# Performance work log

Hardware: AMD Instinct MI355X
Metric: run time of the kernel (lower is better)

## Reference

```python
import jax, jax.numpy as jnp
import numpy as np


def _hilbert_envelope(x1d):
    """|analytic signal| of a real 1-D signal, matching scipy.signal.hilbert."""
    N = x1d.shape[0]  # static at trace time
    h = np.zeros(N, dtype=np.float32)
    if N % 2 == 0:
        h[0] = 1.0
        h[N // 2] = 1.0
        h[1:N // 2] = 2.0
    else:
        h[0] = 1.0
        h[1:(N + 1) // 2] = 2.0
    Xf = jnp.fft.fft(x1d)
    analytic = jnp.fft.ifft(Xf * jnp.asarray(h))
    return jnp.abs(analytic)


def setup_inputs() -> dict:
    key = jax.random.key(0)
    B, L, D = 32, 4096, 64
    x = jax.random.normal(key, (B, L, D), dtype=jnp.float32)
    return {"x": x}


def reference(x):
    B, L, D = x.shape
    flat = x.reshape(-1)  # [B*L*D], one long signal as in the original
    up = jnp.clip(flat, 0.0, None)
    down = jnp.clip(-flat, 0.0, None)
    envelope_max = _hilbert_envelope(up).reshape(B, L, D)
    envelope_min = (-_hilbert_envelope(down)).reshape(B, L, D)
    avg_envelope = (envelope_max + envelope_min) * 0.5
    imf = x - avg_envelope
    # torch.std(dim=1, unbiased=True) -> ddof=1 over the time axis
    std_res = jnp.std(imf, axis=1, keepdims=True, ddof=1) + jnp.float32(0.01)
    return imf / std_res, avg_envelope
```

## Files before the change

### kernel.cpp

```cpp
#include <hip/hip_runtime.h>
#include <math.h>

#define NTOT 8388608
#define N1   2048
#define N2   4096
#define BB   32
#define LL   4096
#define DD   64

enum { M_NONE = 0, M_TW = 1, M_SCALE = 4 };

__device__ inline float2 cmul(float2 a, float2 b) {
    return make_float2(a.x*b.x - a.y*b.y, a.x*b.y + a.y*b.x);
}
__device__ inline float2 cmul_conj(float2 a, float2 b) {
    return make_float2(a.x*b.x + a.y*b.y, a.y*b.x - a.x*b.y);
}
__device__ inline float2 cadd(float2 a, float2 b){ return make_float2(a.x+b.x, a.y+b.y); }
__device__ inline float2 csub(float2 a, float2 b){ return make_float2(a.x-b.x, a.y-b.y); }
__device__ inline float2 mul_pi(float2 a){ return make_float2(-a.y, a.x); }
__device__ inline float2 mul_mi(float2 a){ return make_float2(a.y, -a.x); }
__device__ inline int pidx(int a){ return a + (a >> 4); }

template<bool INV>
__device__ inline void dft8(const float2* x, float2* y) {
    const float C = 0.70710678118654752f;
    float2 t0=cadd(x[0],x[4]), t1=cadd(x[1],x[5]), t2=cadd(x[2],x[6]), t3=cadd(x[3],x[7]);
    float2 u0=csub(x[0],x[4]), u1=csub(x[1],x[5]), u2=csub(x[2],x[6]), u3=csub(x[3],x[7]);
    if (!INV) {
        u1 = make_float2(C*(u1.x+u1.y), C*(u1.y-u1.x));
        u2 = mul_mi(u2);
        u3 = make_float2(C*(u3.y-u3.x), -C*(u3.x+u3.y));
    } else {
        u1 = make_float2(C*(u1.x-u1.y), C*(u1.y+u1.x));
        u2 = mul_pi(u2);
        u3 = make_float2(-C*(u3.x+u3.y), C*(u3.x-u3.y));
    }
    {
        float2 s0=cadd(t0,t2), s1=cadd(t1,t3), d0=csub(t0,t2);
        float2 d1 = INV ? mul_pi(csub(t1,t3)) : mul_mi(csub(t1,t3));
        y[0]=cadd(s0,s1); y[4]=csub(s0,s1); y[2]=cadd(d0,d1); y[6]=csub(d0,d1);
    }
    {
        float2 s0=cadd(u0,u2), s1=cadd(u1,u3), d0=csub(u0,u2);
        float2 d1 = INV ? mul_pi(csub(u1,u3)) : mul_mi(csub(u1,u3));
        y[1]=cadd(s0,s1); y[5]=csub(s0,s1); y[3]=cadd(d0,d1); y[7]=csub(d0,d1);
    }
}

__device__ inline void dft8_h0_inv(const float2* x, float2* y) {
    const float C = 0.70710678118654752f;
    float2 u1 = make_float2(C*(x[1].x - x[1].y), C*(x[1].y + x[1].x));
    float2 u2 = mul_pi(x[2]);
    float2 u3 = make_float2(-C*(x[3].x + x[3].y), C*(x[3].x - x[3].y));
    {
        float2 s0=cadd(x[0],x[2]), s1=cadd(x[1],x[3]), d0=csub(x[0],x[2]);
        float2 d1 = mul_pi(csub(x[1],x[3]));
        y[0]=cadd(s0,s1); y[4]=csub(s0,s1); y[2]=cadd(d0,d1); y[6]=csub(d0,d1);
    }
    {
        float2 s0=cadd(x[0],u2), s1=cadd(u1,u3), d0=csub(x[0],u2);
        float2 d1 = mul_pi(csub(u1,u3));
        y[1]=cadd(s0,s1); y[5]=csub(s0,s1); y[3]=cadd(d0,d1); y[7]=csub(d0,d1);
    }
}

template<bool INV>
__device__ inline void dft4(const float2* u, float2* y) {
    float2 s0=cadd(u[0],u[2]), s1=cadd(u[1],u[3]), d0=csub(u[0],u[2]);
    float2 d1 = INV ? mul_pi(csub(u[1],u[3])) : mul_mi(csub(u[1],u[3]));
    y[0]=cadd(s0,s1); y[2]=csub(s0,s1); y[1]=cadd(d0,d1); y[3]=csub(d0,d1);
}

template<bool INV, int SH>
__device__ inline void twiddle8(float2* y, int ps, const float2* __restrict__ T1t) {
    float2 w1 = T1t[(ps << SH) & 4095];
    float2 w2 = cmul(w1, w1);
    float2 w3 = cmul(w2, w1);
    float2 w4 = cmul(w2, w2);
    float2 w5 = cmul(w4, w1);
    float2 w6 = cmul(w3, w3);
    float2 w7 = cmul(w4, w3);
    if (!INV) {
        y[1]=cmul(y[1],w1); y[2]=cmul(y[2],w2); y[3]=cmul(y[3],w3);
        y[4]=cmul(y[4],w4); y[5]=cmul(y[5],w5); y[6]=cmul(y[6],w6); y[7]=cmul(y[7],w7);
    } else {
        y[1]=cmul_conj(y[1],w1); y[2]=cmul_conj(y[2],w2); y[3]=cmul_conj(y[3],w3);
        y[4]=cmul_conj(y[4],w4); y[5]=cmul_conj(y[5],w5); y[6]=cmul_conj(y[6],w6); y[7]=cmul_conj(y[7],w7);
    }
}

__global__ __launch_bounds__(256) void gen_tables(float2* T1, float2* T2) {
    int j = blockIdx.x * 256 + threadIdx.x;
    if (j < 4096) {
        double ang = -2.0 * M_PI * (double)j / 4096.0;
        T1[j] = make_float2((float)cos(ang), (float)sin(ang));
    } else if (j < 4096 + 2048) {
        int b = j - 4096;
        double ang = -2.0 * M_PI * (double)b / 8388608.0;
        T2[b] = make_float2((float)cos(ang), (float)sin(ang));
    }
}

__device__ inline float2 wbig(int t, const float2* __restrict__ T1t, const float2* __restrict__ T2t) {
    return cmul(T1t[t >> 11], T2t[t & 2047]);
}

template<bool INV, int MODE>
__global__ __launch_bounds__(512) void fft4096(float2* data,
                                               const float2* __restrict__ T1t,
                                               const float2* __restrict__ T2t) {
    __shared__ float2 S[4352];
    const int t = threadIdx.x;
    const int r = blockIdx.x;
    float2* base = data + (size_t)r * 4096;

    float2 x[8], y[8];
    #pragma unroll
    for (int m = 0; m < 8; ++m) x[m] = base[t + 512*m];

    #pragma unroll
    for (int st = 0; st < 3; ++st) {
        const int s = 1 << (3*st);
        const int q = t & (s - 1);
        const int ps = t - q;
        dft8<INV>(x, y);
        twiddle8<INV, 0>(y, ps, T1t);
        if (st) __syncthreads();
        #pragma unroll
        for (int k = 0; k < 8; ++k) S[pidx(8*ps + q + k*s)] = y[k];
        __syncthreads();
        #pragma unroll
        for (int m = 0; m < 8; ++m) x[m] = S[pidx(t + 512*m)];
    }
    dft8<INV>(x, y);

    if (MODE == M_TW) {
        float2 wb    = wbig(r * t, T1t, T2t);
        float2 wstep = wbig(512 * r, T1t, T2t);
        #pragma unroll
        for (int k = 0; k < 8; ++k) {
            int o = t + 512*k;
            base[o] = INV ? cmul_conj(y[k], wb) : cmul(y[k], wb);
            wb = INV ? cmul_conj(wb, wstep) : cmul(wb, wstep);
        }
    } else {
        #pragma unroll
        for (int k = 0; k < 8; ++k) {
            int o = t + 512*k;
            float2 v = y[k];
            if (MODE == M_SCALE) {
                const float sc = 1.f / 8388608.f;
                v.x *= sc; v.y *= sc;
            }
            base[o] = v;
        }
    }
}

__global__ __launch_bounds__(256) void fftmid(float2* data,
                                              const float2* __restrict__ T1t,
                                              const float2* __restrict__ T2t) {
    __shared__ float2 S[2176];
    const int t = threadIdx.x;
    const int r = blockIdx.x;
    float2* base = data + (size_t)r * 2048;

    float2 x[8], y[8];
    #pragma unroll
    for (int m = 0; m < 8; ++m) x[m] = base[t + 256*m];

    #pragma unroll
    for (int st = 0; st < 3; ++st) {
        const int s = 1 << (3*st);
        const int q = t & (s - 1);
        const int ps = t - q;
        dft8<false>(x, y);
        twiddle8<false, 1>(y, ps, T1t);
        if (st) __syncthreads();
        #pragma unroll
        for (int k = 0; k < 8; ++k) S[pidx(8*ps + q + k*s)] = y[k];
        __syncthreads();
        if (st < 2) {
            #pragma unroll
            for (int m = 0; m < 8; ++m) x[m] = S[pidx(t + 256*m)];
        }
    }
    float2 xa[4], xb[4], ya[4], yb[4];
    #pragma unroll
    for (int m = 0; m < 4; ++m) {
        xa[m] = S[pidx(t + 512*m)];
        xb[m] = S[pidx(t + 256 + 512*m)];
    }
    dft4<false>(xa, ya);
    dft4<false>(xb, yb);
    __syncthreads();
    #pragma unroll
    for (int k = 0; k < 4; ++k) {
        int o = t + 512*k;
        if (o < 1024) {
            float h = (o == 0 && r == 0) ? 1.f : 2.f;
            S[pidx(o)] = make_float2(ya[k].x * h, ya[k].y * h);
        } else if (o == 1024) {
            S[pidx(1024)] = (r == 0) ? ya[k] : make_float2(0.f, 0.f);
        }
        int o2 = o + 256;
        if (o2 < 1024) S[pidx(o2)] = make_float2(yb[k].x * 2.f, yb[k].y * 2.f);
    }
    __syncthreads();
    #pragma unroll
    for (int m = 0; m < 4; ++m) x[m] = S[pidx(t + 256*m)];
    dft8_h0_inv(x, y);
    if (t == 0) {
        float2 c = S[pidx(1024)];
        #pragma unroll
        for (int k = 0; k < 8; ++k) {
            if (k & 1) { y[k].x -= c.x; y[k].y -= c.y; }
            else       { y[k].x += c.x; y[k].y += c.y; }
        }
    }
    twiddle8<true, 1>(y, t, T1t);
    __syncthreads();
    #pragma unroll
    for (int k = 0; k < 8; ++k) S[pidx(8*t + k)] = y[k];
    __syncthreads();
    #pragma unroll
    for (int st = 1; st < 3; ++st) {
        const int s = 1 << (3*st);
        const int q = t & (s - 1);
        const int ps = t - q;
        #pragma unroll
        for (int m = 0; m < 8; ++m) x[m] = S[pidx(t + 256*m)];
        dft8<true>(x, y);
        twiddle8<true, 1>(y, ps, T1t);
        __syncthreads();
        #pragma unroll
        for (int k = 0; k < 8; ++k) S[pidx(8*ps + q + k*s)] = y[k];
        __syncthreads();
    }
    #pragma unroll
    for (int m = 0; m < 4; ++m) {
        xa[m] = S[pidx(t + 512*m)];
        xb[m] = S[pidx(t + 256 + 512*m)];
    }
    dft4<true>(xa, ya);
    dft4<true>(xb, yb);
    {
        float2 wka   = wbig(r * t, T1t, T2t);
        float2 w256  = wbig(256 * r, T1t, T2t);
        float2 w512  = cmul(w256, w256);
        float2 wkb   = cmul(wka, w256);
        #pragma unroll
        for (int k = 0; k < 4; ++k) {
            int o = t + 512*k;
            base[o]       = cmul_conj(ya[k], wka);
            base[o + 256] = cmul_conj(yb[k], wkb);
            wka = cmul(wka, w512);
            wkb = cmul(wkb, w512);
        }
    }
}

__global__ __launch_bounds__(256) void k_pre(const float* __restrict__ x, float2* __restrict__ A) {
    __shared__ float tile[32][33];
    int c0 = blockIdx.x * 32;
    int r0 = blockIdx.y * 32;
    int tx = threadIdx.x, ty = threadIdx.y;
    #pragma unroll
    for (int j = 0; j < 32; j += 8)
        tile[ty + j][tx] = x[(size_t)(r0 + ty + j) * N1 + c0 + tx];
    __syncthreads();
    #pragma unroll
    for (int j = 0; j < 32; j += 8) {
        float v = tile[tx][ty + j];
        A[(size_t)(c0 + ty + j) * N2 + r0 + tx] = make_float2(fmaxf(v, 0.f), fmaxf(-v, 0.f));
    }
}

__global__ __launch_bounds__(256) void k_trans(const float2* __restrict__ in, float2* __restrict__ out,
                                               int inCols, int inRows) {
    __shared__ float2 tile[32][33];
    int c0 = blockIdx.x * 32;
    int r0 = blockIdx.y * 32;
    int tx = threadIdx.x, ty = threadIdx.y;
    #pragma unroll
    for (int j = 0; j < 32; j += 8)
        tile[ty + j][tx] = in[(size_t)(r0 + ty + j) * inCols + c0 + tx];
    __syncthreads();
    #pragma unroll
    for (int j = 0; j < 32; j += 8)
        out[(size_t)(c0 + ty + j) * inRows + r0 + tx] = tile[tx][ty + j];
}

__global__ __launch_bounds__(256) void k_post(const float2* __restrict__ A, const float* __restrict__ x,
                                              float* __restrict__ out) {
    __shared__ float2 tile[32][33];
    int c0 = blockIdx.x * 32;
    int r0 = blockIdx.y * 32;
    int tx = threadIdx.x, ty = threadIdx.y;
    #pragma unroll
    for (int j = 0; j < 32; j += 8)
        tile[ty + j][tx] = A[(size_t)(r0 + ty + j) * N2 + c0 + tx];
    __syncthreads();
    #pragma unroll
    for (int j = 0; j < 32; j += 8) {
        int n2 = c0 + ty + j;
        int n1 = r0 + tx;
        size_t n = (size_t)n2 * N1 + n1;
        float2 w = tile[tx][ty + j];
        float xv = x[n];
        float up = fmaxf(xv, 0.f);
        float dn = fmaxf(-xv, 0.f);
        float hu = w.y - dn;
        float hd = up - w.x;
        float em = sqrtf(up*up + hu*hu);
        float en = sqrtf(dn*dn + hd*hd);
        float avg = 0.5f * (em - en);
        out[n]        = xv - avg;
        out[NTOT + n] = avg;
    }
}

__global__ __launch_bounds__(256) void std_partial(const float* __restrict__ imf, float* __restrict__ part) {
    int blk = blockIdx.x;
    int b   = blk >> 4;
    int ch  = blk & 15;
    int d   = threadIdx.x & 63;
    int lw  = threadIdx.x >> 6;
    float s1 = 0.f, s2 = 0.f;
    const float* base = imf + (size_t)b * LL * DD;
    for (int i = 0; i < 64; ++i) {
        int l = ch * 256 + lw * 64 + i;
        float v = base[(size_t)l * DD + d];
        s1 += v;
        s2 += v * v;
    }
    __shared__ float r1[4][64];
    __shared__ float r2[4][64];
    r1[lw][d] = s1; r2[lw][d] = s2;
    __syncthreads();
    if (lw == 0) {
        s1 = r1[0][d] + r1[1][d] + r1[2][d] + r1[3][d];
        s2 = r2[0][d] + r2[1][d] + r2[2][d] + r2[3][d];
        int pi = blk * 64 + d;
        part[pi] = s1;
        part[BB * 16 * 64 + pi] = s2;
    }
}

__global__ __launch_bounds__(256) void std_final(const float* __restrict__ part, float* __restrict__ scalev) {
    int g = blockIdx.x * 256 + threadIdx.x;
    int b = g >> 6, d = g & 63;
    float s1 = 0.f, s2 = 0.f;
    for (int ch = 0; ch < 16; ++ch) {
        int pi = (b * 16 + ch) * 64 + d;
        s1 += part[pi];
        s2 += part[BB * 16 * 64 + pi];
    }
    float mean = s1 / (float)LL;
    float var  = (s2 - (float)LL * mean * mean) / (float)(LL - 1);
    var = fmaxf(var, 0.f);
    scalev[g] = 1.f / (sqrtf(var) + 0.01f);
}

__global__ __launch_bounds__(256) void apply_scale(float* __restrict__ out, const float* __restrict__ scalev) {
    size_t i = ((size_t)blockIdx.x * 256 + threadIdx.x) * 4;
    float4 v = *(float4*)(out + i);
    int b = (int)(i >> 18);
    int d = (int)(i & 63);
    const float* sc = scalev + b * 64;
    v.x *= sc[d];
    v.y *= sc[d + 1];
    v.z *= sc[d + 2];
    v.w *= sc[d + 3];
    *(float4*)(out + i) = v;
}

extern "C" void kernel_launch(void* const* d_in, const int* in_sizes, int n_in,
                              void* d_out, int out_size, void* d_ws, size_t ws_size,
                              hipStream_t stream) {
    const float* x = (const float*)d_in[0];
    float* out = (float*)d_out;
    char* w = (char*)d_ws;

    float2* T1     = (float2*)w;
    float2* T2     = (float2*)(w + 32 * 1024);
    float*  part   = (float*)(w + 48 * 1024);
    float*  scalev = (float*)(w + 320 * 1024);
    float2* A      = (float2*)(w + (1 << 20));
    float2* Bbuf   = (float2*)d_out;

    hipLaunchKernelGGL(gen_tables, dim3(24), dim3(256), 0, stream, T1, T2);

    hipLaunchKernelGGL(k_pre, dim3(N1/32, N2/32), dim3(32, 8), 0, stream, x, A);
    hipLaunchKernelGGL((fft4096<false, M_TW>), dim3(N1), dim3(512), 0, stream, A, T1, T2);
    hipLaunchKernelGGL(k_trans, dim3(N2/32, N1/32), dim3(32, 8), 0, stream, A, Bbuf, N2, N1);
    hipLaunchKernelGGL(fftmid, dim3(N2), dim3(256), 0, stream, Bbuf, T1, T2);
    hipLaunchKernelGGL(k_trans, dim3(N1/32, N2/32), dim3(32, 8), 0, stream, Bbuf, A, N1, N2);
    hipLaunchKernelGGL((fft4096<true, M_SCALE>), dim3(N1), dim3(512), 0, stream, A, T1, T2);
    hipLaunchKernelGGL(k_post, dim3(N2/32, N1/32), dim3(32, 8), 0, stream, A, x, out);

    hipLaunchKernelGGL(std_partial, dim3(BB * 16), dim3(256), 0, stream, out, part);
    hipLaunchKernelGGL(std_final, dim3(8), dim3(256), 0, stream, part, scalev);
    hipLaunchKernelGGL(apply_scale, dim3(NTOT / 4 / 256), dim3(256), 0, stream, out, scalev);
}
```

Before: 201.8 us.

## Replace transpose-based four-step FFT with fused column/row FFT kernels

Restructures the 8M-point Hilbert FFT as a four-step scheme with 2048 rows by 4096 columns. Two column-FFT kernels each process 4 adjacent columns in shared memory with an XOR swizzle, so the separate transpose, pre and post kernels are no longer needed. The row kernel fuses the forward FFT, the Hilbert mask and the inverse FFT in place. This removes several full-array global-memory round trips. In exchange it uses strided float4 column loads and 64KB of shared memory per block, which limits occupancy.

```diff
diff --git a/kernel.cpp b/kernel.cpp
--- a/kernel.cpp
+++ b/kernel.cpp
@@ -2,13 +2,11 @@
 #include <math.h>
 
 #define NTOT 8388608
-#define N1   2048
-#define N2   4096
+#define RR   2048
+#define CC   4096
 #define BB   32
 #define LL   4096
 #define DD   64
-
-enum { M_NONE = 0, M_TW = 1, M_SCALE = 4 };
 
 __device__ inline float2 cmul(float2 a, float2 b) {
     return make_float2(a.x*b.x - a.y*b.y, a.x*b.y + a.y*b.x);
@@ -21,6 +19,7 @@
 __device__ inline float2 mul_pi(float2 a){ return make_float2(-a.y, a.x); }
 __device__ inline float2 mul_mi(float2 a){ return make_float2(a.y, -a.x); }
 __device__ inline int pidx(int a){ return a + (a >> 4); }
+__device__ inline int swz(int a){ return a ^ (((a >> 5) & 15) << 1); }
 
 template<bool INV>
 __device__ inline void dft8(const float2* x, float2* y) {
@@ -106,218 +105,234 @@
     return cmul(T1t[t >> 11], T2t[t & 2047]);
 }
 
-template<bool INV, int MODE>
-__global__ __launch_bounds__(512) void fft4096(float2* data,
+__global__ __launch_bounds__(256) void col_fwd(const float* __restrict__ x, float2* __restrict__ Y,
+                                               const float2* __restrict__ T1t,
+                                               const float2* __restrict__ T2t) {
+    __shared__ float2 S[8192];
+    const int t = threadIdx.x;
+    const int c0 = blockIdx.x * 4;
+    #pragma unroll
+    for (int g = 0; g < 8; ++g) {
+        int n1 = t + 256*g;
+        float4 v = *(const float4*)(x + (size_t)n1*CC + c0);
+        S[swz(4*n1+0)] = make_float2(fmaxf(v.x,0.f), fmaxf(-v.x,0.f));
+        S[swz(4*n1+1)] = make_float2(fmaxf(v.y,0.f), fmaxf(-v.y,0.f));
+        S[swz(4*n1+2)] = make_float2(fmaxf(v.z,0.f), fmaxf(-v.z,0.f));
+        S[swz(4*n1+3)] = make_float2(fmaxf(v.w,0.f), fmaxf(-v.w,0.f));
+    }
+    __syncthreads();
+    const int u = t >> 2, c = t & 3;
+    const int n2 = c0 + c;
+    float2 in[4][8], y[8];
+    #pragma unroll
+    for (int st = 0; st < 3; ++st) {
+        const int s = 1 << (3*st);
+        #pragma unroll
+        for (int g = 0; g < 4; ++g) {
+            int j = u + 64*g;
+            #pragma unroll
+            for (int m = 0; m < 8; ++m) in[g][m] = S[swz(4*(j + 256*m) + c)];
+        }
+        __syncthreads();
+        #pragma unroll
+        for (int g = 0; g < 4; ++g) {
+            int j = u + 64*g;
+            int q = j & (s-1), ps = j - q;
+            dft8<false>(in[g], y);
+            twiddle8<false,1>(y, ps, T1t);
+            #pragma unroll
+            for (int k = 0; k < 8; ++k) S[swz(4*(8*ps + q + k*s) + c)] = y[k];
+        }
+        __syncthreads();
+    }
+    float2 q4[8][4];
+    #pragma unroll
+    for (int g = 0; g < 8; ++g) {
+        int j = u + 64*g;
+        #pragma unroll
+        for (int m = 0; m < 4; ++m) q4[g][m] = S[swz(4*(j + 512*m) + c)];
+    }
+    __syncthreads();
+    const float2 ws = wbig(512 * n2, T1t, T2t);
+    #pragma unroll
+    for (int g = 0; g < 8; ++g) {
+        int j = u + 64*g;
+        float2 y4[4];
+        dft4<false>(q4[g], y4);
+        float2 wb = wbig(n2 * j, T1t, T2t);
+        #pragma unroll
+        for (int m = 0; m < 4; ++m) {
+            S[swz(4*(j + 512*m) + c)] = cmul(y4[m], wb);
+            wb = cmul(wb, ws);
+        }
+    }
+    __syncthreads();
+    #pragma unroll
+    for (int g = 0; g < 8; ++g) {
+        int k1 = t + 256*g;
+        float2 a = S[swz(4*k1+0)], b = S[swz(4*k1+1)];
+        float2 cc2 = S[swz(4*k1+2)], d = S[swz(4*k1+3)];
+        float4* p = (float4*)(Y + (size_t)k1*CC + c0);
+        p[0] = make_float4(a.x, a.y, b.x, b.y);
+        p[1] = make_float4(cc2.x, cc2.y, d.x, d.y);
+    }
+}
+
+__global__ __launch_bounds__(512) void row_mid(float2* __restrict__ Y,
                                                const float2* __restrict__ T1t,
                                                const float2* __restrict__ T2t) {
     __shared__ float2 S[4352];
     const int t = threadIdx.x;
     const int r = blockIdx.x;
-    float2* base = data + (size_t)r * 4096;
-
-    float2 x[8], y[8];
-    #pragma unroll
-    for (int m = 0; m < 8; ++m) x[m] = base[t + 512*m];
-
+    float2* base = Y + (size_t)r * CC;
+    float2 x8[8], y8[8];
+    #pragma unroll
+    for (int m = 0; m < 8; ++m) x8[m] = base[t + 512*m];
     #pragma unroll
     for (int st = 0; st < 3; ++st) {
         const int s = 1 << (3*st);
-        const int q = t & (s - 1);
-        const int ps = t - q;
-        dft8<INV>(x, y);
-        twiddle8<INV, 0>(y, ps, T1t);
+        const int q = t & (s-1), ps = t - q;
+        dft8<false>(x8, y8);
+        twiddle8<false,0>(y8, ps, T1t);
         if (st) __syncthreads();
         #pragma unroll
-        for (int k = 0; k < 8; ++k) S[pidx(8*ps + q + k*s)] = y[k];
-        __syncthreads();
-        #pragma unroll
-        for (int m = 0; m < 8; ++m) x[m] = S[pidx(t + 512*m)];
-    }
-    dft8<INV>(x, y);
-
-    if (MODE == M_TW) {
-        float2 wb    = wbig(r * t, T1t, T2t);
-        float2 wstep = wbig(512 * r, T1t, T2t);
+        for (int k = 0; k < 8; ++k) S[pidx(8*ps + q + k*s)] = y8[k];
+        __syncthreads();
+        #pragma unroll
+        for (int m = 0; m < 8; ++m) x8[m] = S[pidx(t + 512*m)];
+    }
+    dft8<false>(x8, y8);
+    float2 z8[4];
+    #pragma unroll
+    for (int k = 0; k < 4; ++k) {
+        int k2 = t + 512*k;
+        float h = (k2 == 0 && r == 0) ? 1.f : 2.f;
+        z8[k] = make_float2(y8[k].x*h, y8[k].y*h);
+    }
+    float2 corner = y8[4];
+    dft8_h0_inv(z8, y8);
+    if (r == 0 && t == 0) {
         #pragma unroll
         for (int k = 0; k < 8; ++k) {
-            int o = t + 512*k;
-            base[o] = INV ? cmul_conj(y[k], wb) : cmul(y[k], wb);
-            wb = INV ? cmul_conj(wb, wstep) : cmul(wb, wstep);
-        }
-    } else {
-        #pragma unroll
-        for (int k = 0; k < 8; ++k) {
-            int o = t + 512*k;
-            float2 v = y[k];
-            if (MODE == M_SCALE) {
-                const float sc = 1.f / 8388608.f;
-                v.x *= sc; v.y *= sc;
-            }
-            base[o] = v;
-        }
-    }
-}
-
-__global__ __launch_bounds__(256) void fftmid(float2* data,
-                                              const float2* __restrict__ T1t,
-                                              const float2* __restrict__ T2t) {
-    __shared__ float2 S[2176];
+            if (k & 1) { y8[k].x -= corner.x; y8[k].y -= corner.y; }
+            else       { y8[k].x += corner.x; y8[k].y += corner.y; }
+        }
+    }
+    twiddle8<true,0>(y8, t, T1t);
+    __syncthreads();
+    #pragma unroll
+    for (int k = 0; k < 8; ++k) S[pidx(8*t + k)] = y8[k];
+    __syncthreads();
+    #pragma unroll
+    for (int st = 1; st < 3; ++st) {
+        const int s = 1 << (3*st);
+        const int q = t & (s-1), ps = t - q;
+        #pragma unroll
+        for (int m = 0; m < 8; ++m) x8[m] = S[pidx(t + 512*m)];
+        dft8<true>(x8, y8);
+        twiddle8<true,0>(y8, ps, T1t);
+        __syncthreads();
+        #pragma unroll
+        for (int k = 0; k < 8; ++k) S[pidx(8*ps + q + k*s)] = y8[k];
+        __syncthreads();
+    }
+    #pragma unroll
+    for (int m = 0; m < 8; ++m) x8[m] = S[pidx(t + 512*m)];
+    dft8<true>(x8, y8);
+    const float sc = 1.f / 8388608.f;
+    float2 wb = wbig(r * t, T1t, T2t);
+    wb.x *= sc; wb.y *= sc;
+    const float2 wstep = wbig(512 * r, T1t, T2t);
+    #pragma unroll
+    for (int k = 0; k < 8; ++k) {
+        base[t + 512*k] = cmul_conj(y8[k], wb);
+        wb = cmul(wb, wstep);
+    }
+}
+
+__global__ __launch_bounds__(256) void col_inv(const float2* __restrict__ Y, const float* __restrict__ x,
+                                               float* __restrict__ out,
+                                               const float2* __restrict__ T1t,
+                                               const float2* __restrict__ T2t) {
+    __shared__ float2 S[8192];
     const int t = threadIdx.x;
-    const int r = blockIdx.x;
-    float2* base = data + (size_t)r * 2048;
-
-    float2 x[8], y[8];
-    #pragma unroll
-    for (int m = 0; m < 8; ++m) x[m] = base[t + 256*m];
-
+    const int c0 = blockIdx.x * 4;
+    #pragma unroll
+    for (int g = 0; g < 8; ++g) {
+        int k1 = t + 256*g;
+        const float4* p = (const float4*)(Y + (size_t)k1*CC + c0);
+        float4 ab = p[0], cd = p[1];
+        S[swz(4*k1+0)] = make_float2(ab.x, ab.y);
+        S[swz(4*k1+1)] = make_float2(ab.z, ab.w);
+        S[swz(4*k1+2)] = make_float2(cd.x, cd.y);
+        S[swz(4*k1+3)] = make_float2(cd.z, cd.w);
+    }
+    __syncthreads();
+    const int u = t >> 2, c = t & 3;
+    float2 in[4][8], y[8];
     #pragma unroll
     for (int st = 0; st < 3; ++st) {
         const int s = 1 << (3*st);
-        const int q = t & (s - 1);
-        const int ps = t - q;
-        dft8<false>(x, y);
-        twiddle8<false, 1>(y, ps, T1t);
-        if (st) __syncthreads();
-        #pragma unroll
-        for (int k = 0; k < 8; ++k) S[pidx(8*ps + q + k*s)] = y[k];
-        __syncthreads();
-        if (st < 2) {
+        #pragma unroll
+        for (int g = 0; g < 4; ++g) {
+            int j = u + 64*g;
             #pragma unroll
-            for (int m = 0; m < 8; ++m) x[m] = S[pidx(t + 256*m)];
-        }
-    }
-    float2 xa[4], xb[4], ya[4], yb[4];
-    #pragma unroll
-    for (int m = 0; m < 4; ++m) {
-        xa[m] = S[pidx(t + 512*m)];
-        xb[m] = S[pidx(t + 256 + 512*m)];
-    }
-    dft4<false>(xa, ya);
-    dft4<false>(xb, yb);
-    __syncthreads();
-    #pragma unroll
-    for (int k = 0; k < 4; ++k) {
-        int o = t + 512*k;
-        if (o < 1024) {
-            float h = (o == 0 && r == 0) ? 1.f : 2.f;
-            S[pidx(o)] = make_float2(ya[k].x * h, ya[k].y * h);
-        } else if (o == 1024) {
-            S[pidx(1024)] = (r == 0) ? ya[k] : make_float2(0.f, 0.f);
-        }
-        int o2 = o + 256;
-        if (o2 < 1024) S[pidx(o2)] = make_float2(yb[k].x * 2.f, yb[k].y * 2.f);
-    }
-    __syncthreads();
-    #pragma unroll
-    for (int m = 0; m < 4; ++m) x[m] = S[pidx(t + 256*m)];
-    dft8_h0_inv(x, y);
-    if (t == 0) {
-        float2 c = S[pidx(1024)];
-        #pragma unroll
-        for (int k = 0; k < 8; ++k) {
-            if (k & 1) { y[k].x -= c.x; y[k].y -= c.y; }
-            else       { y[k].x += c.x; y[k].y += c.y; }
-        }
-    }
-    twiddle8<true, 1>(y, t, T1t);
-    __syncthreads();
-    #pragma unroll
-    for (int k = 0; k < 8; ++k) S[pidx(8*t + k)] = y[k];
-    __syncthreads();
-    #pragma unroll
-    for (int st = 1; st < 3; ++st) {
-        const int s = 1 << (3*st);
-        const int q = t & (s - 1);
-        const int ps = t - q;
-        #pragma unroll
-        for (int m = 0; m < 8; ++m) x[m] = S[pidx(t + 256*m)];
-        dft8<true>(x, y);
-        twiddle8<true, 1>(y, ps, T1t);
-        __syncthreads();
-        #pragma unroll
-        for (int k = 0; k < 8; ++k) S[pidx(8*ps + q + k*s)] = y[k];
-        __syncthreads();
-    }
-    #pragma unroll
-    for (int m = 0; m < 4; ++m) {
-        xa[m] = S[pidx(t + 512*m)];
-        xb[m] = S[pidx(t + 256 + 512*m)];
-    }
-    dft4<true>(xa, ya);
-    dft4<true>(xb, yb);
-    {
-        float2 wka   = wbig(r * t, T1t, T2t);
-        float2 w256  = wbig(256 * r, T1t, T2t);
-        float2 w512  = cmul(w256, w256);
-        float2 wkb   = cmul(wka, w256);
-        #pragma unroll
-        for (int k = 0; k < 4; ++k) {
-            int o = t + 512*k;
-            base[o]       = cmul_conj(ya[k], wka);
-            base[o + 256] = cmul_conj(yb[k], wkb);
-            wka = cmul(wka, w512);
-            wkb = cmul(wkb, w512);
-        }
-    }
-}
-
-__global__ __launch_bounds__(256) void k_pre(const float* __restrict__ x, float2* __restrict__ A) {
-    __shared__ float tile[32][33];
-    int c0 = blockIdx.x * 32;
-    int r0 = blockIdx.y * 32;
-    int tx = threadIdx.x, ty = threadIdx.y;
-    #pragma unroll
-    for (int j = 0; j < 32; j += 8)
-        tile[ty + j][tx] = x[(size_t)(r0 + ty + j) * N1 + c0 + tx];
-    __syncthreads();
-    #pragma unroll
-    for (int j = 0; j < 32; j += 8) {
-        float v = tile[tx][ty + j];
-        A[(size_t)(c0 + ty + j) * N2 + r0 + tx] = make_float2(fmaxf(v, 0.f), fmaxf(-v, 0.f));
-    }
-}
-
-__global__ __launch_bounds__(256) void k_trans(const float2* __restrict__ in, float2* __restrict__ out,
-                                               int inCols, int inRows) {
-    __shared__ float2 tile[32][33];
-    int c0 = blockIdx.x * 32;
-    int r0 = blockIdx.y * 32;
-    int tx = threadIdx.x, ty = threadIdx.y;
-    #pragma unroll
-    for (int j = 0; j < 32; j += 8)
-        tile[ty + j][tx] = in[(size_t)(r0 + ty + j) * inCols + c0 + tx];
-    __syncthreads();
-    #pragma unroll
-    for (int j = 0; j < 32; j += 8)
-        out[(size_t)(c0 + ty + j) * inRows + r0 + tx] = tile[tx][ty + j];
-}
-
-__global__ __launch_bounds__(256) void k_post(const float2* __restrict__ A, const float* __restrict__ x,
-                                              float* __restrict__ out) {
-    __shared__ float2 tile[32][33];
-    int c0 = blockIdx.x * 32;
-    int r0 = blockIdx.y * 32;
-    int tx = threadIdx.x, ty = threadIdx.y;
-    #pragma unroll
-    for (int j = 0; j < 32; j += 8)
-        tile[ty + j][tx] = A[(size_t)(r0 + ty + j) * N2 + c0 + tx];
-    __syncthreads();
-    #pragma unroll
-    for (int j = 0; j < 32; j += 8) {
-        int n2 = c0 + ty + j;
-        int n1 = r0 + tx;
-        size_t n = (size_t)n2 * N1 + n1;
-        float2 w = tile[tx][ty + j];
-        float xv = x[n];
-        float up = fmaxf(xv, 0.f);
-        float dn = fmaxf(-xv, 0.f);
-        float hu = w.y - dn;
-        float hd = up - w.x;
-        float em = sqrtf(up*up + hu*hu);
-        float en = sqrtf(dn*dn + hd*hd);
-        float avg = 0.5f * (em - en);
-        out[n]        = xv - avg;
-        out[NTOT + n] = avg;
+            for (int m = 0; m < 8; ++m) in[g][m] = S[swz(4*(j + 256*m) + c)];
+        }
+        __syncthreads();
+        #pragma unroll
+        for (int g = 0; g < 4; ++g) {
+            int j = u + 64*g;
+            int q = j & (s-1), ps = j - q;
+            dft8<true>(in[g], y);
+            twiddle8<true,1>(y, ps, T1t);
+            #pragma unroll
+            for (int k = 0; k < 8; ++k) S[swz(4*(8*ps + q + k*s) + c)] = y[k];
+        }
+        __syncthreads();
+    }
+    float2 q4[8][4];
+    #pragma unroll
+    for (int g = 0; g < 8; ++g) {
+        int j = u + 64*g;
+        #pragma unroll
+        for (int m = 0; m < 4; ++m) q4[g][m] = S[swz(4*(j + 512*m) + c)];
+    }
+    __syncthreads();
+    #pragma unroll
+    for (int g = 0; g < 8; ++g) {
+        int j = u + 64*g;
+        float2 y4[4];
+        dft4<true>(q4[g], y4);
+        #pragma unroll
+        for (int m = 0; m < 4; ++m) S[swz(4*(j + 512*m) + c)] = y4[m];
+    }
+    __syncthreads();
+    #pragma unroll
+    for (int g = 0; g < 8; ++g) {
+        int n1 = t + 256*g;
+        size_t n = (size_t)n1*CC + c0;
+        float4 xv = *(const float4*)(x + n);
+        float2 w0 = S[swz(4*n1+0)], w1 = S[swz(4*n1+1)];
+        float2 w2 = S[swz(4*n1+2)], w3 = S[swz(4*n1+3)];
+        float4 imf, avg;
+        {
+            float up, dn, hu, hd, em, en, a;
+            up = fmaxf(xv.x,0.f); dn = fmaxf(-xv.x,0.f); hu = w0.y - dn; hd = up - w0.x;
+            em = sqrtf(up*up+hu*hu); en = sqrtf(dn*dn+hd*hd); a = 0.5f*(em-en);
+            imf.x = xv.x - a; avg.x = a;
+            up = fmaxf(xv.y,0.f); dn = fmaxf(-xv.y,0.f); hu = w1.y - dn; hd = up - w1.x;
+            em = sqrtf(up*up+hu*hu); en = sqrtf(dn*dn+hd*hd); a = 0.5f*(em-en);
+            imf.y = xv.y - a; avg.y = a;
+            up = fmaxf(xv.z,0.f); dn = fmaxf(-xv.z,0.f); hu = w2.y - dn; hd = up - w2.x;
+            em = sqrtf(up*up+hu*hu); en = sqrtf(dn*dn+hd*hd); a = 0.5f*(em-en);
+            imf.z = xv.z - a; avg.z = a;
+            up = fmaxf(xv.w,0.f); dn = fmaxf(-xv.w,0.f); hu = w3.y - dn; hd = up - w3.x;
+            em = sqrtf(up*up+hu*hu); en = sqrtf(dn*dn+hd*hd); a = 0.5f*(em-en);
+            imf.w = xv.w - a; avg.w = a;
+        }
+        *(float4*)(out + n) = imf;
+        *(float4*)(out + NTOT + n) = avg;
     }
 }
 
@@ -387,18 +402,13 @@
     float2* T2     = (float2*)(w + 32 * 1024);
     float*  part   = (float*)(w + 48 * 1024);
     float*  scalev = (float*)(w + 320 * 1024);
-    float2* A      = (float2*)(w + (1 << 20));
-    float2* Bbuf   = (float2*)d_out;
+    float2* Y      = (float2*)(w + (1 << 20));
 
     hipLaunchKernelGGL(gen_tables, dim3(24), dim3(256), 0, stream, T1, T2);
 
-    hipLaunchKernelGGL(k_pre, dim3(N1/32, N2/32), dim3(32, 8), 0, stream, x, A);
-    hipLaunchKernelGGL((fft4096<false, M_TW>), dim3(N1), dim3(512), 0, stream, A, T1, T2);
-    hipLaunchKernelGGL(k_trans, dim3(N2/32, N1/32), dim3(32, 8), 0, stream, A, Bbuf, N2, N1);
-    hipLaunchKernelGGL(fftmid, dim3(N2), dim3(256), 0, stream, Bbuf, T1, T2);
-    hipLaunchKernelGGL(k_trans, dim3(N1/32, N2/32), dim3(32, 8), 0, stream, Bbuf, A, N1, N2);
-    hipLaunchKernelGGL((fft4096<true, M_SCALE>), dim3(N1), dim3(512), 0, stream, A, T1, T2);
-    hipLaunchKernelGGL(k_post, dim3(N2/32, N1/32), dim3(32, 8), 0, stream, A, x, out);
+    hipLaunchKernelGGL(col_fwd, dim3(CC/4), dim3(256), 0, stream, x, Y, T1, T2);
+    hipLaunchKernelGGL(row_mid, dim3(RR),   dim3(512), 0, stream, Y, T1, T2);
+    hipLaunchKernelGGL(col_inv, dim3(CC/4), dim3(256), 0, stream, Y, x, out, T1, T2);
 
     hipLaunchKernelGGL(std_partial, dim3(BB * 16), dim3(256), 0, stream, out, part);
     hipLaunchKernelGGL(std_final, dim3(8), dim3(256), 0, stream, part, scalev);
```

After: 269.1 us. 33.4% more time.

## Fuse std partial sums into k_post and recompute imf in final scale pass

Applied to the files above, without the earlier changes.

k_post now accumulates per-column sum and sum-of-squares of imf and writes block partials, so the separate std_partial pass that reread the 32 MB imf array goes away. imf is no longer stored. The final kernel recomputes it from x and the stored envelope, then scales it. Partials are placed in the first half of the output buffer, which later gets overwritten. This removes one full read pass and one write pass. In exchange, std_final has more partials to reduce and the last pass reads two arrays instead of one.

```diff
diff --git a/kernel.cpp b/kernel.cpp
--- a/kernel.cpp
+++ b/kernel.cpp
@@ -293,8 +293,9 @@
 }
 
 __global__ __launch_bounds__(256) void k_post(const float2* __restrict__ A, const float* __restrict__ x,
-                                              float* __restrict__ out) {
+                                              float* __restrict__ out, float* __restrict__ part) {
     __shared__ float2 tile[32][33];
+    __shared__ float red[2][8][32];
     int c0 = blockIdx.x * 32;
     int r0 = blockIdx.y * 32;
     int tx = threadIdx.x, ty = threadIdx.y;
@@ -302,6 +303,7 @@
     for (int j = 0; j < 32; j += 8)
         tile[ty + j][tx] = A[(size_t)(r0 + ty + j) * N2 + c0 + tx];
     __syncthreads();
+    float s1 = 0.f, s2 = 0.f;
     #pragma unroll
     for (int j = 0; j < 32; j += 8) {
         int n2 = c0 + ty + j;
@@ -316,46 +318,36 @@
         float em = sqrtf(up*up + hu*hu);
         float en = sqrtf(dn*dn + hd*hd);
         float avg = 0.5f * (em - en);
-        out[n]        = xv - avg;
+        float imf = xv - avg;
         out[NTOT + n] = avg;
-    }
-}
-
-__global__ __launch_bounds__(256) void std_partial(const float* __restrict__ imf, float* __restrict__ part) {
-    int blk = blockIdx.x;
-    int b   = blk >> 4;
-    int ch  = blk & 15;
-    int d   = threadIdx.x & 63;
-    int lw  = threadIdx.x >> 6;
-    float s1 = 0.f, s2 = 0.f;
-    const float* base = imf + (size_t)b * LL * DD;
-    for (int i = 0; i < 64; ++i) {
-        int l = ch * 256 + lw * 64 + i;
-        float v = base[(size_t)l * DD + d];
-        s1 += v;
-        s2 += v * v;
-    }
-    __shared__ float r1[4][64];
-    __shared__ float r2[4][64];
-    r1[lw][d] = s1; r2[lw][d] = s2;
-    __syncthreads();
-    if (lw == 0) {
-        s1 = r1[0][d] + r1[1][d] + r1[2][d] + r1[3][d];
-        s2 = r2[0][d] + r2[1][d] + r2[2][d] + r2[3][d];
-        int pi = blk * 64 + d;
-        part[pi] = s1;
-        part[BB * 16 * 64 + pi] = s2;
+        s1 += imf;
+        s2 += imf * imf;
+    }
+    red[0][ty][tx] = s1;
+    red[1][ty][tx] = s2;
+    __syncthreads();
+    if (ty == 0) {
+        #pragma unroll
+        for (int e = 1; e < 8; ++e) { s1 += red[0][e][tx]; s2 += red[1][e][tx]; }
+        int slot = blockIdx.y * 128 + blockIdx.x;
+        part[slot * 32 + tx]          = s1;
+        part[262144 + slot * 32 + tx] = s2;
     }
 }
 
 __global__ __launch_bounds__(256) void std_final(const float* __restrict__ part, float* __restrict__ scalev) {
     int g = blockIdx.x * 256 + threadIdx.x;
     int b = g >> 6, d = g & 63;
+    int dh = d >> 5, dl = d & 31;
     float s1 = 0.f, s2 = 0.f;
-    for (int ch = 0; ch < 16; ++ch) {
-        int pi = (b * 16 + ch) * 64 + d;
-        s1 += part[pi];
-        s2 += part[BB * 16 * 64 + pi];
+    for (int lq = 0; lq < 32; ++lq) {
+        int by = lq * 2 + dh;
+        #pragma unroll
+        for (int ch = 0; ch < 4; ++ch) {
+            int slot = by * 128 + b * 4 + ch;
+            s1 += part[slot * 32 + dl];
+            s2 += part[262144 + slot * 32 + dl];
+        }
     }
     float mean = s1 / (float)LL;
     float var  = (s2 - (float)LL * mean * mean) / (float)(LL - 1);
@@ -363,16 +355,19 @@
     scalev[g] = 1.f / (sqrtf(var) + 0.01f);
 }
 
-__global__ __launch_bounds__(256) void apply_scale(float* __restrict__ out, const float* __restrict__ scalev) {
+__global__ __launch_bounds__(256) void imf_final(const float* __restrict__ x, float* __restrict__ out,
+                                                 const float* __restrict__ scalev) {
     size_t i = ((size_t)blockIdx.x * 256 + threadIdx.x) * 4;
-    float4 v = *(float4*)(out + i);
+    float4 xv = *(const float4*)(x + i);
+    float4 av = *(const float4*)(out + NTOT + i);
     int b = (int)(i >> 18);
     int d = (int)(i & 63);
     const float* sc = scalev + b * 64;
-    v.x *= sc[d];
-    v.y *= sc[d + 1];
-    v.z *= sc[d + 2];
-    v.w *= sc[d + 3];
+    float4 v;
+    v.x = (xv.x - av.x) * sc[d];
+    v.y = (xv.y - av.y) * sc[d + 1];
+    v.z = (xv.z - av.z) * sc[d + 2];
+    v.w = (xv.w - av.w) * sc[d + 3];
     *(float4*)(out + i) = v;
 }
 
@@ -385,10 +380,10 @@
 
     float2* T1     = (float2*)w;
     float2* T2     = (float2*)(w + 32 * 1024);
-    float*  part   = (float*)(w + 48 * 1024);
-    float*  scalev = (float*)(w + 320 * 1024);
+    float*  scalev = (float*)(w + 48 * 1024);
     float2* A      = (float2*)(w + (1 << 20));
     float2* Bbuf   = (float2*)d_out;
+    float*  part   = (float*)d_out;
 
     hipLaunchKernelGGL(gen_tables, dim3(24), dim3(256), 0, stream, T1, T2);
 
@@ -398,9 +393,8 @@
     hipLaunchKernelGGL(fftmid, dim3(N2), dim3(256), 0, stream, Bbuf, T1, T2);
     hipLaunchKernelGGL(k_trans, dim3(N1/32, N2/32), dim3(32, 8), 0, stream, Bbuf, A, N1, N2);
     hipLaunchKernelGGL((fft4096<true, M_SCALE>), dim3(N1), dim3(512), 0, stream, A, T1, T2);
-    hipLaunchKernelGGL(k_post, dim3(N2/32, N1/32), dim3(32, 8), 0, stream, A, x, out);
-
-    hipLaunchKernelGGL(std_partial, dim3(BB * 16), dim3(256), 0, stream, out, part);
+
+    hipLaunchKernelGGL(k_post, dim3(N2/32, N1/32), dim3(32, 8), 0, stream, A, x, out, part);
     hipLaunchKernelGGL(std_final, dim3(8), dim3(256), 0, stream, part, scalev);
-    hipLaunchKernelGGL(apply_scale, dim3(NTOT / 4 / 256), dim3(256), 0, stream, out, scalev);
-}
+    hipLaunchKernelGGL(imf_final, dim3(NTOT / 4 / 256), dim3(256), 0, stream, x, out, scalev);
+}
```

New measurement: 203.7 us. About the same (+1.0%).
